# Kernel tuning notes

Measured on AMD Instinct MI355X. Metric: run time of the kernel, lower is better.

## Reference

```python
import jax, jax.numpy as jnp
import numpy as np

N_HEADS = 16
N_EMBD = 1024
HEAD_DIM = N_EMBD // N_HEADS
WINDOW = 512
B, T = 2, 2048


def setup_inputs() -> dict:
    key = jax.random.key(0)
    ks = jax.random.split(key, 5)
    s = 0.02
    return {
        "x": jax.random.normal(ks[0], (B, T, N_EMBD), dtype=jnp.float32),
        "Wq": jax.random.normal(ks[1], (N_EMBD, N_EMBD), dtype=jnp.float32) * s,
        "Wk": jax.random.normal(ks[2], (N_EMBD, N_EMBD), dtype=jnp.float32) * s,
        "Wv": jax.random.normal(ks[3], (N_EMBD, N_EMBD), dtype=jnp.float32) * s,
        "Wo": jax.random.normal(ks[4], (N_EMBD, N_EMBD), dtype=jnp.float32) * s,
    }


def _sliding_window_mask(T, window):
    # mask[i, j] True iff max(0, i-window+1) <= j <= i  (causal banded)
    i = jnp.arange(T)[:, None]
    j = jnp.arange(T)[None, :]
    return (j <= i) & (j > i - window)


def reference(x, Wq, Wk, Wv, Wo):
    Bb, Tt, C = x.shape
    # nn.Linear applies x @ W.T; we store W as [in, out] so just x @ W
    def heads(w):
        return (x @ w).reshape(Bb, Tt, N_HEADS, HEAD_DIM).transpose(0, 2, 1, 3)
    q, k, v = heads(Wq), heads(Wk), heads(Wv)  # [B, H, T, D]
    scores = jnp.einsum("bhqd,bhkd->bhqk", q, k) / jnp.sqrt(jnp.float32(HEAD_DIM))
    mask = _sliding_window_mask(Tt, WINDOW)  # [T, T]
    scores = jnp.where(mask[None, None], scores, jnp.float32(-jnp.inf))
    attn = jax.nn.softmax(scores, axis=-1)
    out = jnp.einsum("bhqk,bhkd->bhqd", attn, v)  # [B, H, T, D]
    out = out.transpose(0, 2, 1, 3).reshape(Bb, Tt, C)
    return out @ Wo
```

## Files before the change

### kernel.cpp

```cpp
#include <hip/hip_runtime.h>

#define B_SZ 2
#define T_SZ 2048
#define C_SZ 1024
#define K_SZ 1024
#define QKV_LD 3072
#define H_CNT 16
#define D_SZ 64
#define WIN 512

typedef __bf16 bf16_t;
typedef bf16_t bf16x8 __attribute__((ext_vector_type(8)));
typedef bf16_t bf16x4 __attribute__((ext_vector_type(4)));
typedef float f32x4 __attribute__((ext_vector_type(4)));
typedef unsigned int u32;

__device__ __forceinline__ f32x4 mfma16(bf16x8 a, bf16x8 b, f32x4 c) {
  return __builtin_amdgcn_mfma_f32_16x16x32_bf16(a, b, c, 0, 0, 0);
}

__device__ __forceinline__ void gload_lds16(const void* gsrc, void* ldst) {
  auto g = (__attribute__((address_space(1))) void*)(unsigned long long)gsrc;
  auto l = (__attribute__((address_space(3))) void*)(unsigned int)(unsigned long long)ldst;
  __builtin_amdgcn_global_load_lds(g, l, 16, 0, 0);
}

__global__ __launch_bounds__(256) void prep(
    const float* __restrict__ x, bf16_t* __restrict__ xb,
    const float* __restrict__ W0, const float* __restrict__ W1,
    const float* __restrict__ W2, const float* __restrict__ W3,
    bf16_t* __restrict__ T0, bf16_t* __restrict__ T1,
    bf16_t* __restrict__ T2, bf16_t* __restrict__ T3) {
  if (blockIdx.z == 4) {
    const int base = (blockIdx.y * 32 + blockIdx.x) * 256 + threadIdx.x;
#pragma unroll
    for (int j = 0; j < 4; ++j) {
      const int idx = base + j * 262144;
      const float4 v = ((const float4*)x)[idx];
      bf16x4 r;
      r[0] = (bf16_t)v.x; r[1] = (bf16_t)v.y; r[2] = (bf16_t)v.z; r[3] = (bf16_t)v.w;
      ((bf16x4*)xb)[idx] = r;
    }
    return;
  }
  __shared__ float tile[32][33];
  const float* W = blockIdx.z == 0 ? W0 : blockIdx.z == 1 ? W1 : blockIdx.z == 2 ? W2 : W3;
  bf16_t* Tt = blockIdx.z == 0 ? T0 : blockIdx.z == 1 ? T1 : blockIdx.z == 2 ? T2 : T3;
  const int tx = threadIdx.x & 31, ty = threadIdx.x >> 5;
  const int r0 = blockIdx.y * 32, c0 = blockIdx.x * 32;
#pragma unroll
  for (int i = 0; i < 4; ++i)
    tile[ty + i * 8][tx] = W[(size_t)(r0 + ty + i * 8) * C_SZ + c0 + tx];
  __syncthreads();
#pragma unroll
  for (int i = 0; i < 4; ++i)
    Tt[(size_t)(c0 + ty + i * 8) * C_SZ + r0 + tx] = (bf16_t)tile[tx][ty + i * 8];
}

#define GM_NT 16

__global__ __launch_bounds__(1024, 4) void gemm256(
    const bf16_t* __restrict__ A, const bf16_t* __restrict__ Bt,
    bf16_t* __restrict__ C, bf16_t* __restrict__ Vt) {
  __shared__ __align__(16) bf16_t As[2][256 * 64];
  __shared__ __align__(16) bf16_t Bs[2][192 * 64];
  const int wg = blockIdx.x + 16 * blockIdx.y;
  const int swz = (wg & 7) * 32 + (wg >> 3);
  const int bx = swz & 15, by = swz >> 4;
  const int m0 = by * 256, n0 = bx * 192;
  const int tid = threadIdx.x, w = tid >> 6, lane = tid & 63;
  const int wr = w >> 2, wc = w & 3;
  const int g = lane >> 4, l15 = lane & 15, sw = l15 & 7;
  const int srow = lane >> 3, sj = lane & 7;

  f32x4 acc[4][3] = {};

  auto stageA = [&](int buf, int half, int k0) {
    const int rg = w * 8;
    gload_lds16(A + (size_t)(m0 + half * 128 + rg + srow) * K_SZ + k0 + ((sj ^ srow) << 3),
                &As[buf][half * 8192 + rg * 64]);
  };
  auto stageB = [&](int buf, int part, int k0) {
    const int grp = part == 0 ? w : 16 + w;
    const int rg = grp * 8;
    gload_lds16(Bt + (size_t)(n0 + rg + srow) * K_SZ + k0 + ((sj ^ srow) << 3),
                &Bs[buf][rg * 64]);
  };

  stageA(0, 0, 0); stageA(0, 1, 0);
  stageB(0, 0, 0);
  if (w < 8) stageB(0, 1, 0);

#define LDAF(MF, KK) \
  (*(const bf16x8*)&As[buf][(wr * 64 + (MF) * 16 + l15) * 64 + \
                            ((((KK) << 2) | g) ^ sw) * 8])
#define LDBF(NF, KK) \
  (*(const bf16x8*)&Bs[buf][(wc * 48 + (NF) * 16 + l15) * 64 + \
                            ((((KK) << 2) | g) ^ sw) * 8])
#define MROW(MF, AF)                              \
  acc[(MF)][0] = mfma16(AF, b0, acc[(MF)][0]);    \
  acc[(MF)][1] = mfma16(AF, b1, acc[(MF)][1]);    \
  acc[(MF)][2] = mfma16(AF, b2, acc[(MF)][2]);

#pragma unroll 2
  for (int t = 0; t < GM_NT; ++t) {
    const int buf = t & 1, nb = buf ^ 1;
    const int k1 = (t + 1) * 64;
    asm volatile("s_waitcnt vmcnt(0)" ::: "memory");
    __builtin_amdgcn_s_barrier();

    {
      bf16x8 a0 = LDAF(0, 0), a1 = LDAF(1, 0), a2 = LDAF(2, 0), a3 = LDAF(3, 0);
      bf16x8 b0 = LDBF(0, 0), b1 = LDBF(1, 0), b2 = LDBF(2, 0);
      if (t < GM_NT - 1) { stageA(nb, 0, k1); stageA(nb, 1, k1); }
      __builtin_amdgcn_s_barrier();
      __builtin_amdgcn_s_setprio(1);
      MROW(0, a0) MROW(1, a1) MROW(2, a2) MROW(3, a3)
      __builtin_amdgcn_s_setprio(0);
      __builtin_amdgcn_s_barrier();
    }
    {
      bf16x8 a0 = LDAF(0, 1), a1 = LDAF(1, 1), a2 = LDAF(2, 1), a3 = LDAF(3, 1);
      bf16x8 b0 = LDBF(0, 1), b1 = LDBF(1, 1), b2 = LDBF(2, 1);
      if (t < GM_NT - 1) {
        stageB(nb, 0, k1);
        if (w < 8) stageB(nb, 1, k1);
      }
      __builtin_amdgcn_s_barrier();
      __builtin_amdgcn_s_setprio(1);
      MROW(0, a0) MROW(1, a1) MROW(2, a2) MROW(3, a3)
      __builtin_amdgcn_s_setprio(0);
    }
  }

#pragma unroll
  for (int mf = 0; mf < 4; ++mf) {
    const int row = m0 + wr * 64 + mf * 16 + g * 4;
#pragma unroll
    for (int nf = 0; nf < 3; ++nf) {
      const int colb = n0 + wc * 48 + nf * 16;
      if (colb >= 2048) {
        const int d = colb - 2048 + l15;
        const size_t vo =
            ((size_t)((row >> 11) * 16 + (d >> 6)) * 64 + (d & 63)) * (size_t)T_SZ +
            (row & (T_SZ - 1));
        union { bf16_t h4[4]; uint2 u; } pk;
#pragma unroll
        for (int i = 0; i < 4; ++i) pk.h4[i] = (bf16_t)acc[mf][nf][i];
        *(uint2*)(Vt + vo) = pk.u;
      } else {
#pragma unroll
        for (int i = 0; i < 4; ++i)
          C[(size_t)(row + i) * QKV_LD + colb + l15] = (bf16_t)acc[mf][nf][i];
      }
    }
  }
}

__global__ __launch_bounds__(256, 3) void gemm128(
    const bf16_t* __restrict__ A, int lda, const bf16_t* __restrict__ Bt,
    float* __restrict__ C, int N) {
  __shared__ __align__(16) bf16_t As[2][128 * 64];
  __shared__ __align__(16) bf16_t Bs[2][64 * 64];
  const int wg = blockIdx.x + 16 * blockIdx.y;
  const int swz = (wg & 7) * 64 + (wg >> 3);
  const int bx = swz & 15, by = swz >> 4;
  const int m0 = by * 128, n0 = bx * 64;
  const int tid = threadIdx.x, w = tid >> 6, lane = tid & 63;
  const int wr = w >> 1, wc = w & 1;
  const int g = lane >> 4, l15 = lane & 15, sw = l15 & 7;
  const int srow = lane >> 3, sj = lane & 7;

  f32x4 acc[4][2] = {};

  auto stage = [&](int buf, int k0) {
#pragma unroll
    for (int r = 0; r < 4; ++r) {
      const int rg = (w * 4 + r) * 8;
      gload_lds16(A + (size_t)(m0 + rg + srow) * lda + k0 + ((sj ^ srow) << 3),
                  &As[buf][rg * 64]);
    }
#pragma unroll
    for (int r = 0; r < 2; ++r) {
      const int rg = (w * 2 + r) * 8;
      gload_lds16(Bt + (size_t)(n0 + rg + srow) * K_SZ + k0 + ((sj ^ srow) << 3),
                  &Bs[buf][rg * 64]);
    }
  };

  stage(0, 0);

#pragma unroll 2
  for (int t = 0; t < GM_NT; ++t) {
    const int buf = t & 1;
    asm volatile("s_waitcnt vmcnt(0)" ::: "memory");
    __builtin_amdgcn_s_barrier();
    if (t < GM_NT - 1) stage(buf ^ 1, (t + 1) * 64);
#pragma unroll
    for (int kk = 0; kk < 2; ++kk) {
      bf16x8 af[4], bfr[2];
#pragma unroll
      for (int mf = 0; mf < 4; ++mf)
        af[mf] = *(const bf16x8*)&As[buf][(wr * 64 + mf * 16 + l15) * 64 +
                                          (((kk << 2) | g) ^ sw) * 8];
#pragma unroll
      for (int nf = 0; nf < 2; ++nf)
        bfr[nf] = *(const bf16x8*)&Bs[buf][(wc * 32 + nf * 16 + l15) * 64 +
                                           (((kk << 2) | g) ^ sw) * 8];
      __builtin_amdgcn_s_setprio(1);
#pragma unroll
      for (int mf = 0; mf < 4; ++mf)
#pragma unroll
        for (int nf = 0; nf < 2; ++nf)
          acc[mf][nf] = mfma16(af[mf], bfr[nf], acc[mf][nf]);
      __builtin_amdgcn_s_setprio(0);
    }
    __builtin_amdgcn_s_barrier();
  }

#pragma unroll
  for (int mf = 0; mf < 4; ++mf)
#pragma unroll
    for (int nf = 0; nf < 2; ++nf)
#pragma unroll
      for (int i = 0; i < 4; ++i)
        C[(size_t)(m0 + wr * 64 + mf * 16 + g * 4 + i) * N +
          n0 + wc * 32 + nf * 16 + l15] = acc[mf][nf][i];
}

__global__ __launch_bounds__(512) void attn_kernel(
    bf16_t* __restrict__ QKV, const bf16_t* __restrict__ Vt) {
  __shared__ __align__(16) bf16_t Kl[2][64 * 64];
  __shared__ __align__(16) bf16_t Vl[2][64 * 64];

  const int qt = ((blockIdx.x & 7) << 1) | (blockIdx.x >> 3);
  const int bh = blockIdx.y;
  const int b = bh >> 4, h = bh & 15;
  const int q0 = qt * 128;
  const int tid = threadIdx.x, w = tid >> 6, lane = tid & 63;
  const int g = lane >> 4, l15 = lane & 15, gh = g >> 1;
  const int wrow0 = q0 + w * 16;
  const int myrow = wrow0 + l15;
  const int sub = lane >> 3, jj = lane & 7;
  const int sw = l15 & 7;

  auto stage = [&](int bufi, int kt) {
    const int row = w * 8 + sub;
    const int sj = jj ^ sub;
    gload_lds16(QKV + ((size_t)b * T_SZ + kt + row) * QKV_LD + 1024 + h * D_SZ + sj * 8,
                &Kl[bufi][w * 512]);
    gload_lds16(Vt + ((size_t)bh * D_SZ + row) * T_SZ + kt + sj * 8,
                &Vl[bufi][w * 512]);
  };

  bf16x8 qf[2];
  {
    const bf16_t* qptr = QKV + ((size_t)b * T_SZ + myrow) * QKV_LD + h * D_SZ;
    const float QSC = 0.125f * 1.44269504f;
#pragma unroll
    for (int c2 = 0; c2 < 2; ++c2) {
      bf16x8 t = *(const bf16x8*)(qptr + c2 * 32 + g * 8);
      bf16x8 o;
#pragma unroll
      for (int j = 0; j < 8; ++j) o[j] = (bf16_t)((float)t[j] * QSC);
      qf[c2] = o;
    }
  }

  float m_s = -1e30f, l_s = 0.f;
  f32x4 oacc[4] = {};

  int kstart = q0 - (WIN - 1);
  if (kstart < 0) kstart = 0;
  kstart &= ~63;
  const int nt = (q0 + 128 - kstart) >> 6;

  stage(0, kstart);

  for (int it = 0; it < nt; ++it) {
    const int kt = kstart + (it << 6);
    const int cur = it & 1;
    if (it + 1 < nt) {
      stage(cur ^ 1, kt + 64);
      asm volatile("s_waitcnt vmcnt(2)" ::: "memory");
    } else {
      asm volatile("s_waitcnt vmcnt(0)" ::: "memory");
    }
    __builtin_amdgcn_s_barrier();
    __builtin_amdgcn_sched_barrier(0);

    const bool skip = (kt + 63 < wrow0 - (WIN - 1)) || (kt > wrow0 + 15);
    if (!skip) {
      f32x4 s[4] = {};
#pragma unroll
      for (int t = 0; t < 4; ++t) {
        const bf16_t* kbase = &Kl[cur][(t * 16 + l15) * 64];
#pragma unroll
        for (int c2 = 0; c2 < 2; ++c2) {
          const bf16x8 kf = *(const bf16x8*)(kbase + (((c2 * 4 + g) ^ sw) << 3));
          s[t] = mfma16(kf, qf[c2], s[t]);
        }
      }

      const bool interior = (kt + 63 <= wrow0) && (kt >= wrow0 + 15 - (WIN - 1));
      float sv[4][4];
      if (interior) {
#pragma unroll
        for (int t = 0; t < 4; ++t)
#pragma unroll
          for (int i = 0; i < 4; ++i) sv[t][i] = s[t][i];
      } else {
#pragma unroll
        for (int t = 0; t < 4; ++t)
#pragma unroll
          for (int i = 0; i < 4; ++i) {
            const int kk = kt + t * 16 + g * 4 + i;
            sv[t][i] = (kk <= myrow && kk > myrow - WIN) ? s[t][i] : -1e30f;
          }
      }

      float mx = sv[0][0];
#pragma unroll
      for (int t = 0; t < 4; ++t)
#pragma unroll
        for (int i = 0; i < 4; ++i)
          if (t || i) mx = fmaxf(mx, sv[t][i]);
      mx = fmaxf(mx, __shfl_xor(mx, 16));
      mx = fmaxf(mx, __shfl_xor(mx, 32));

      float mbase;
      const bool defer = __all((mx <= m_s + 8.f) && (m_s > -1e29f));
      if (defer) {
        mbase = m_s;
      } else {
        const float mnew = fmaxf(m_s, mx);
        const float scl = exp2f(m_s - mnew);
        m_s = mnew;
        mbase = (mnew > -1e29f) ? mnew : 1e30f;
        float sc4[4];
#pragma unroll
        for (int i = 0; i < 4; ++i) sc4[i] = __shfl(scl, g * 4 + i, 16);
#pragma unroll
        for (int c = 0; c < 4; ++c)
#pragma unroll
          for (int i = 0; i < 4; ++i) oacc[c][i] *= sc4[i];
        l_s *= scl;
      }

      float p[4][4];
      float rsum = 0.f;
#pragma unroll
      for (int t = 0; t < 4; ++t)
#pragma unroll
        for (int i = 0; i < 4; ++i) {
          p[t][i] = exp2f(sv[t][i] - mbase);
          rsum += p[t][i];
        }
      rsum += __shfl_xor(rsum, 16);
      rsum += __shfl_xor(rsum, 32);
      l_s += rsum;

      u32 Wp[4][2];
#pragma unroll
      for (int t = 0; t < 4; ++t)
#pragma unroll
        for (int w2 = 0; w2 < 2; ++w2) {
          union { bf16_t hh[2]; u32 uu; } pk;
          pk.hh[0] = (bf16_t)p[t][2 * w2];
          pk.hh[1] = (bf16_t)p[t][2 * w2 + 1];
          Wp[t][w2] = pk.uu;
        }

#pragma unroll
      for (int kp = 0; kp < 2; ++kp) {
        const u32 lo0 = Wp[2 * kp][0], lo1 = Wp[2 * kp][1];
        const u32 hi0 = Wp[2 * kp + 1][0], hi1 = Wp[2 * kp + 1][1];
        union { u32 u[4]; bf16x8 v; } pa;
        pa.u[0] = gh ? hi0 : lo0;
        pa.u[1] = gh ? hi1 : lo1;
        pa.u[2] = (u32)__shfl_xor((int)(gh ? lo0 : hi0), 32);
        pa.u[3] = (u32)__shfl_xor((int)(gh ? lo1 : hi1), 32);

        const int tA = 2 * kp + gh;
        const int low = (g & 1) * 4;
        const int cA = ((tA * 2 + gh) ^ sw) << 3;
        const int cB = ((tA * 2 + (gh ^ 1)) ^ sw) << 3;
#pragma unroll
        for (int c = 0; c < 4; ++c) {
          const bf16_t* vbase = &Vl[cur][(c * 16 + l15) * 64];
          union { bf16x4 h[2]; bf16x8 v; } vv;
          vv.h[0] = *(const bf16x4*)(vbase + cA + low);
          vv.h[1] = *(const bf16x4*)(vbase + cB + low);
          oacc[c] = mfma16(pa.v, vv.v, oacc[c]);
        }
      }
    }
    __builtin_amdgcn_sched_barrier(0);
    __builtin_amdgcn_s_barrier();
  }

  const float invl = 1.0f / l_s;
  float inv4[4];
#pragma unroll
  for (int i = 0; i < 4; ++i) inv4[i] = __shfl(invl, g * 4 + i, 16);
#pragma unroll
  for (int i = 0; i < 4; ++i) {
    const size_t ro = ((size_t)b * T_SZ + wrow0 + g * 4 + i) * QKV_LD + 2048 + h * D_SZ;
#pragma unroll
    for (int c = 0; c < 4; ++c)
      QKV[ro + c * 16 + l15] = (bf16_t)(oacc[c][i] * inv4[i]);
  }
}

extern "C" void kernel_launch(void* const* d_in, const int* in_sizes, int n_in,
                              void* d_out, int out_size, void* d_ws, size_t ws_size,
                              hipStream_t stream) {
  const float* x = (const float*)d_in[0];
  const float* Wq = (const float*)d_in[1];
  const float* Wk = (const float*)d_in[2];
  const float* Wv = (const float*)d_in[3];
  const float* Wo = (const float*)d_in[4];
  float* out = (float*)d_out;
  char* ws = (char*)d_ws;
  const size_t MB = 1ull << 20;
  bf16_t* xb = (bf16_t*)(ws);
  bf16_t* QKVb = (bf16_t*)(ws + 8 * MB);
  bf16_t* WqT = (bf16_t*)(ws + 32 * MB);
  bf16_t* WkT = (bf16_t*)(ws + 34 * MB);
  bf16_t* WvT = (bf16_t*)(ws + 36 * MB);
  bf16_t* WoT = (bf16_t*)(ws + 38 * MB);
  bf16_t* Vtp = (bf16_t*)(ws + 48 * MB);

  prep<<<dim3(32, 32, 5), 256, 0, stream>>>(x, xb, Wq, Wk, Wv, Wo,
                                            WqT, WkT, WvT, WoT);
  gemm256<<<dim3(16, 16), 1024, 0, stream>>>(xb, WqT, QKVb, Vtp);
  attn_kernel<<<dim3(16, B_SZ * H_CNT), 512, 0, stream>>>(QKVb, Vtp);
  gemm128<<<dim3(16, 32), 256, 0, stream>>>(QKVb + 2048, QKV_LD, WoT, out, C_SZ);
}
```

Measured before the change: 86.17 us.

## Triple-buffer B tiles in QKV GEMM and drop redundant barriers across kernels

The QKV GEMM now keeps three LDS buffers for the B operand and prefetches two tiles ahead. Only 12 waves load B, while every wave loads two A row groups. Fine-grained vmcnt waits replace the full drain, and the two intra-iteration barriers are removed. The output GEMM and attention kernel now issue the next-tile prefetch right after the top-of-loop barrier and drop the trailing barrier, halving synchronisation per iteration. Both GEMM loops are fully unrolled. The risks are higher LDS use, lower occupancy, more code size, and reliance on barrier ordering for buffer reuse correctness.

```diff
diff --git a/kernel.cpp b/kernel.cpp
--- a/kernel.cpp
+++ b/kernel.cpp
@@ -63,7 +63,7 @@
     const bf16_t* __restrict__ A, const bf16_t* __restrict__ Bt,
     bf16_t* __restrict__ C, bf16_t* __restrict__ Vt) {
   __shared__ __align__(16) bf16_t As[2][256 * 64];
-  __shared__ __align__(16) bf16_t Bs[2][192 * 64];
+  __shared__ __align__(16) bf16_t Bs[3][192 * 64];
   const int wg = blockIdx.x + 16 * blockIdx.y;
   const int swz = (wg & 7) * 32 + (wg >> 3);
   const int bx = swz & 15, by = swz >> 4;
@@ -75,58 +75,66 @@
 
   f32x4 acc[4][3] = {};
 
-  auto stageA = [&](int buf, int half, int k0) {
-    const int rg = w * 8;
-    gload_lds16(A + (size_t)(m0 + half * 128 + rg + srow) * K_SZ + k0 + ((sj ^ srow) << 3),
-                &As[buf][half * 8192 + rg * 64]);
+  auto stageA = [&](int buf, int k0) {
+#pragma unroll
+    for (int q8 = 0; q8 < 2; ++q8) {
+      const int rg = w * 16 + q8 * 8;
+      gload_lds16(A + (size_t)(m0 + rg + srow) * K_SZ + k0 + ((sj ^ srow) << 3),
+                  &As[buf][rg * 64]);
+    }
   };
-  auto stageB = [&](int buf, int part, int k0) {
-    const int grp = part == 0 ? w : 16 + w;
-    const int rg = grp * 8;
-    gload_lds16(Bt + (size_t)(n0 + rg + srow) * K_SZ + k0 + ((sj ^ srow) << 3),
-                &Bs[buf][rg * 64]);
+  auto stageB = [&](int buf, int k0) {
+#pragma unroll
+    for (int q8 = 0; q8 < 2; ++q8) {
+      const int rg = w * 16 + q8 * 8;
+      gload_lds16(Bt + (size_t)(n0 + rg + srow) * K_SZ + k0 + ((sj ^ srow) << 3),
+                  &Bs[buf][rg * 64]);
+    }
   };
 
-  stageA(0, 0, 0); stageA(0, 1, 0);
-  stageB(0, 0, 0);
-  if (w < 8) stageB(0, 1, 0);
+  if (w < 12) stageB(0, 0);
+  stageA(0, 0);
+  if (w < 12) stageB(1, 64);
 
 #define LDAF(MF, KK) \
   (*(const bf16x8*)&As[buf][(wr * 64 + (MF) * 16 + l15) * 64 + \
                             ((((KK) << 2) | g) ^ sw) * 8])
 #define LDBF(NF, KK) \
-  (*(const bf16x8*)&Bs[buf][(wc * 48 + (NF) * 16 + l15) * 64 + \
-                            ((((KK) << 2) | g) ^ sw) * 8])
+  (*(const bf16x8*)&Bs[bB][(wc * 48 + (NF) * 16 + l15) * 64 + \
+                           ((((KK) << 2) | g) ^ sw) * 8])
 #define MROW(MF, AF)                              \
   acc[(MF)][0] = mfma16(AF, b0, acc[(MF)][0]);    \
   acc[(MF)][1] = mfma16(AF, b1, acc[(MF)][1]);    \
   acc[(MF)][2] = mfma16(AF, b2, acc[(MF)][2]);
 
-#pragma unroll 2
+#pragma unroll
   for (int t = 0; t < GM_NT; ++t) {
     const int buf = t & 1, nb = buf ^ 1;
+    const int bB = t % 3;
     const int k1 = (t + 1) * 64;
-    asm volatile("s_waitcnt vmcnt(0)" ::: "memory");
+    if (t < GM_NT - 1) {
+      if (w < 12) {
+        asm volatile("s_waitcnt vmcnt(2)" ::: "memory");
+      } else {
+        asm volatile("s_waitcnt vmcnt(0)" ::: "memory");
+      }
+    } else {
+      asm volatile("s_waitcnt vmcnt(0)" ::: "memory");
+    }
     __builtin_amdgcn_s_barrier();
 
     {
       bf16x8 a0 = LDAF(0, 0), a1 = LDAF(1, 0), a2 = LDAF(2, 0), a3 = LDAF(3, 0);
       bf16x8 b0 = LDBF(0, 0), b1 = LDBF(1, 0), b2 = LDBF(2, 0);
-      if (t < GM_NT - 1) { stageA(nb, 0, k1); stageA(nb, 1, k1); }
-      __builtin_amdgcn_s_barrier();
+      if (t < GM_NT - 1) stageA(nb, k1);
       __builtin_amdgcn_s_setprio(1);
       MROW(0, a0) MROW(1, a1) MROW(2, a2) MROW(3, a3)
       __builtin_amdgcn_s_setprio(0);
-      __builtin_amdgcn_s_barrier();
     }
     {
       bf16x8 a0 = LDAF(0, 1), a1 = LDAF(1, 1), a2 = LDAF(2, 1), a3 = LDAF(3, 1);
       bf16x8 b0 = LDBF(0, 1), b1 = LDBF(1, 1), b2 = LDBF(2, 1);
-      if (t < GM_NT - 1) {
-        stageB(nb, 0, k1);
-        if (w < 8) stageB(nb, 1, k1);
-      }
-      __builtin_amdgcn_s_barrier();
+      if (t < GM_NT - 2 && w < 12) stageB((t + 2) % 3, (t + 2) * 64);
       __builtin_amdgcn_s_setprio(1);
       MROW(0, a0) MROW(1, a1) MROW(2, a2) MROW(3, a3)
       __builtin_amdgcn_s_setprio(0);
@@ -190,7 +198,7 @@
 
   stage(0, 0);
 
-#pragma unroll 2
+#pragma unroll
   for (int t = 0; t < GM_NT; ++t) {
     const int buf = t & 1;
     asm volatile("s_waitcnt vmcnt(0)" ::: "memory");
@@ -215,7 +223,6 @@
           acc[mf][nf] = mfma16(af[mf], bfr[nf], acc[mf][nf]);
       __builtin_amdgcn_s_setprio(0);
     }
-    __builtin_amdgcn_s_barrier();
   }
 
 #pragma unroll
@@ -280,14 +287,10 @@
   for (int it = 0; it < nt; ++it) {
     const int kt = kstart + (it << 6);
     const int cur = it & 1;
-    if (it + 1 < nt) {
-      stage(cur ^ 1, kt + 64);
-      asm volatile("s_waitcnt vmcnt(2)" ::: "memory");
-    } else {
-      asm volatile("s_waitcnt vmcnt(0)" ::: "memory");
-    }
+    asm volatile("s_waitcnt vmcnt(0)" ::: "memory");
     __builtin_amdgcn_s_barrier();
     __builtin_amdgcn_sched_barrier(0);
+    if (it + 1 < nt) stage(cur ^ 1, kt + 64);
 
     const bool skip = (kt + 63 < wrow0 - (WIN - 1)) || (kt > wrow0 + 15);
     if (!skip) {
@@ -396,7 +399,6 @@
       }
     }
     __builtin_amdgcn_sched_barrier(0);
-    __builtin_amdgcn_s_barrier();
   }
 
   const float invl = 1.0f / l_s;
```

After: 82.16 us. -4.7%, faster.
